# Kernel optimization log

Measured on AMD Instinct MI355X. Metric: run time of the kernel, lower is better.

Reference implementation:

```python
import jax, jax.numpy as jnp
import numpy as np

B, L, D = 4, 4096, 256


def setup_inputs() -> dict:
    key = jax.random.key(0)
    k_x, k_q, k_k, k_v, k_w, k_b = jax.random.split(key, 6)
    s = 1.0 / np.sqrt(D)
    return {
        "x": jax.random.normal(k_x, (B, L, D), dtype=jnp.float32),
        "Wq": jax.random.normal(k_q, (D, D), dtype=jnp.float32) * s,   # nn.Linear weight (out,in)
        "Wk": jax.random.normal(k_k, (D, D), dtype=jnp.float32) * s,
        "Wv": jax.random.normal(k_v, (D, D), dtype=jnp.float32) * s,
        "w_mlp": jax.random.normal(k_w, (D,), dtype=jnp.float32) * s,  # Linear(D,1) weight
        "b_mlp": jnp.zeros((), dtype=jnp.float32),                     # Linear(D,1) bias
    }


def reference(x, Wq, Wk, Wv, w_mlp, b_mlp):
    # Projections (nn.Linear: y = x @ W.T, no bias)
    Q = jnp.einsum("bld,ed->ble", x, Wq)
    K = jnp.einsum("bld,ed->ble", x, Wk)
    V = jnp.einsum("bld,ed->ble", x, Wv)
    # score[b,i,j] = relu((Q[b,i]-K[b,j]) @ w_mlp + b_mlp)
    # decomposed: (Q-K)@w = Q@w - K@w  (exact same math, no (B,L,L,D) tensor)
    q_s = Q @ w_mlp  # (B,L)
    k_s = K @ w_mlp  # (B,L)
    scores = jax.nn.relu(q_s[:, :, None] - k_s[:, None, :] + b_mlp)  # (B,L,L)
    attn = jax.nn.softmax(scores, axis=-1)  # softmax over key axis j
    # out[b,i,d] = sum_j attn[b,i,j] * V[b,j,d]
    out = jnp.einsum("bij,bjd->bid", attn, V)
    return out  # dropout p=0.0 is identity
```

## Files before the change

### kernel.cpp

```cpp
#include <hip/hip_runtime.h>
#include <math.h>

#define BB 4
#define LL 4096
#define DD 256
#define NROWS (BB*LL)
#define CHUNK 32
#define NC (LL/CHUNK)
#define NB 8192

typedef __bf16 bf16x8 __attribute__((ext_vector_type(8)));
typedef __bf16 bf16x4 __attribute__((ext_vector_type(4)));
typedef float floatx4 __attribute__((ext_vector_type(4)));

__global__ void k_prep(const float* __restrict__ Wq, const float* __restrict__ Wk,
                       const float* __restrict__ Wv, const float* __restrict__ w,
                       float* __restrict__ u,
                       __bf16* __restrict__ Wh, __bf16* __restrict__ Wl) {
    __shared__ float wl[16];
    int d = threadIdx.x;
    int e0 = blockIdx.x * 16;
    if (d < 16) wl[d] = w[e0 + d];
    __syncthreads();
    float aq = 0.f, ak = 0.f;
    #pragma unroll
    for (int j = 0; j < 16; ++j) {
        float we = wl[j];
        aq = fmaf(Wq[(size_t)(e0 + j)*DD + d], we, aq);
        ak = fmaf(Wk[(size_t)(e0 + j)*DD + d], we, ak);
        float wv = Wv[(size_t)(e0 + j)*DD + d];
        __bf16 h = (__bf16)wv;
        Wh[(size_t)(e0 + j)*DD + d] = h;
        Wl[(size_t)(e0 + j)*DD + d] = (__bf16)(wv - (float)h);
    }
    atomicAdd(&u[d], aq);
    atomicAdd(&u[DD + d], ak);
}

__global__ void __launch_bounds__(256) k_gemm_mfma(
        const float* __restrict__ x,
        const __bf16* __restrict__ Wh, const __bf16* __restrict__ Wl,
        const float* __restrict__ u, const float* __restrict__ bmlp,
        float* __restrict__ V, float* __restrict__ a, float* __restrict__ c) {
    __shared__ __bf16 Ah[32*40];
    __shared__ __bf16 Al[32*40];
    __shared__ float4 ul[128];
    __shared__ float pros[512];
    const int tid = threadIdx.x;
    const int wave = tid >> 6, lane = tid & 63;
    const int rowBase = blockIdx.x * 32;
    const int quad = lane >> 4, l16 = lane & 15;
    const int srow = tid >> 3, skq = (tid & 7) * 4;

    if (tid < 128) ul[tid] = ((const float4*)u)[tid];

    floatx4 acc[2][4];
    #pragma unroll
    for (int rt = 0; rt < 2; ++rt)
        #pragma unroll
        for (int ct = 0; ct < 4; ++ct)
            acc[rt][ct] = (floatx4){0.f, 0.f, 0.f, 0.f};
    float aq = 0.f, ak = 0.f;

    for (int k0 = 0; k0 < DD; k0 += 32) {
        __syncthreads();
        float4 xv = *(const float4*)(x + (size_t)(rowBase + srow)*DD + k0 + skq);
        __bf16 h0 = (__bf16)xv.x, h1 = (__bf16)xv.y, h2 = (__bf16)xv.z, h3 = (__bf16)xv.w;
        bf16x4 hv = {h0, h1, h2, h3};
        bf16x4 lv = {(__bf16)(xv.x - (float)h0), (__bf16)(xv.y - (float)h1),
                     (__bf16)(xv.z - (float)h2), (__bf16)(xv.w - (float)h3)};
        *(bf16x4*)&Ah[srow*40 + skq] = hv;
        *(bf16x4*)&Al[srow*40 + skq] = lv;
        float4 q4 = ul[(k0 >> 2) + (tid & 7)];
        float4 k4 = ul[64 + (k0 >> 2) + (tid & 7)];
        aq = fmaf(xv.x, q4.x, fmaf(xv.y, q4.y, fmaf(xv.z, q4.z, fmaf(xv.w, q4.w, aq))));
        ak = fmaf(xv.x, k4.x, fmaf(xv.y, k4.y, fmaf(xv.z, k4.z, fmaf(xv.w, k4.w, ak))));
        __syncthreads();
        bf16x8 ah[2], al[2];
        #pragma unroll
        for (int rt = 0; rt < 2; ++rt) {
            int m = rt*16 + l16;
            ah[rt] = *(bf16x8*)&Ah[m*40 + quad*8];
            al[rt] = *(bf16x8*)&Al[m*40 + quad*8];
        }
        #pragma unroll
        for (int ct = 0; ct < 4; ++ct) {
            int n = wave*64 + ct*16 + l16;
            bf16x8 bh = *(const bf16x8*)(Wh + (size_t)n*DD + k0 + quad*8);
            bf16x8 bl = *(const bf16x8*)(Wl + (size_t)n*DD + k0 + quad*8);
            #pragma unroll
            for (int rt = 0; rt < 2; ++rt) {
                acc[rt][ct] = __builtin_amdgcn_mfma_f32_16x16x32_bf16(ah[rt], bh, acc[rt][ct], 0, 0, 0);
                acc[rt][ct] = __builtin_amdgcn_mfma_f32_16x16x32_bf16(ah[rt], bl, acc[rt][ct], 0, 0, 0);
                acc[rt][ct] = __builtin_amdgcn_mfma_f32_16x16x32_bf16(al[rt], bh, acc[rt][ct], 0, 0, 0);
            }
        }
    }
    #pragma unroll
    for (int rt = 0; rt < 2; ++rt)
        #pragma unroll
        for (int ct = 0; ct < 4; ++ct)
            #pragma unroll
            for (int i = 0; i < 4; ++i) {
                int row = rowBase + rt*16 + quad*4 + i;
                int col = wave*64 + ct*16 + l16;
                V[(size_t)row*DD + col] = acc[rt][ct][i];
            }
    __syncthreads();
    pros[tid] = aq;
    pros[256 + tid] = ak;
    __syncthreads();
    if (tid < 32) {
        float sa = 0.f, sc = 0.f;
        #pragma unroll
        for (int j = 0; j < 8; ++j) {
            sa += pros[tid*8 + j];
            sc += pros[256 + tid*8 + j];
        }
        a[rowBase + tid] = sa + bmlp[0];
        c[rowBase + tid] = sc;
    }
}

__global__ void __launch_bounds__(1024) k_sortish(const float* __restrict__ c,
        int* __restrict__ binstart_g, int* __restrict__ perm,
        float* __restrict__ c_sorted, float* __restrict__ e_sorted,
        float* __restrict__ SE, float* __restrict__ hdr) {
    __shared__ float cl[LL];
    __shared__ int   hist[NB];
    __shared__ float esl[LL];
    __shared__ float scrf[64];
    int b = blockIdx.x, tid = threadIdx.x;
    int wave = tid >> 6, lane = tid & 63;
    int* scri = (int*)scrf;

    float4 cv = ((const float4*)(c + (size_t)b*LL))[tid];
    ((float4*)cl)[tid] = cv;
    float cw[4] = {cv.x, cv.y, cv.z, cv.w};
    float mn = fminf(fminf(cw[0],cw[1]), fminf(cw[2],cw[3]));
    float mx = fmaxf(fmaxf(cw[0],cw[1]), fmaxf(cw[2],cw[3]));
    #pragma unroll
    for (int off = 32; off > 0; off >>= 1) {
        mn = fminf(mn, __shfl_down(mn, off));
        mx = fmaxf(mx, __shfl_down(mx, off));
    }
    if (lane == 0) { scrf[wave] = mn; scrf[32 + wave] = mx; }
    __syncthreads();
    if (wave == 0) {
        float m = (lane < 16) ? scrf[lane]      :  3.4e38f;
        float M = (lane < 16) ? scrf[32 + lane] : -3.4e38f;
        #pragma unroll
        for (int off = 32; off > 0; off >>= 1) {
            m = fminf(m, __shfl_down(m, off));
            M = fmaxf(M, __shfl_down(M, off));
        }
        if (lane == 0) { scrf[0] = m; scrf[1] = M; }
    }
    __syncthreads();
    float cmin = scrf[0], cmax = scrf[1];
    float scale = (float)NB / fmaxf(cmax - cmin, 1e-20f);
    __syncthreads();

    ((int4*)hist)[tid] = make_int4(0,0,0,0);
    ((int4*)hist)[tid + 1024] = make_int4(0,0,0,0);
    __syncthreads();

    int bins[4];
    #pragma unroll
    for (int u = 0; u < 4; ++u) {
        int bi = (int)((cw[u] - cmin) * scale);
        bi = bi < 0 ? 0 : (bi > NB-1 ? NB-1 : bi);
        bins[u] = bi;
        atomicAdd(&hist[bi], 1);
    }
    __syncthreads();

    int loc[8]; int base = 0;
    #pragma unroll
    for (int j = 0; j < 8; ++j) { loc[j] = base; base += hist[tid*8 + j]; }
    int incl = base;
    #pragma unroll
    for (int off = 1; off < 64; off <<= 1) {
        int t = __shfl_up(incl, off);
        if (lane >= off) incl += t;
    }
    if (lane == 63) scri[wave] = incl;
    __syncthreads();
    if (wave == 0) {
        int v = (lane < 16) ? scri[lane] : 0;
        int s = v;
        #pragma unroll
        for (int off = 1; off < 16; off <<= 1) {
            int t = __shfl_up(s, off);
            if (lane >= off) s += t;
        }
        if (lane < 16) scri[lane] = s - v;
    }
    __syncthreads();
    int thread_excl = (incl - base) + scri[wave];
    __syncthreads();
    #pragma unroll
    for (int j = 0; j < 8; ++j) {
        int bs = thread_excl + loc[j];
        binstart_g[(size_t)b*(NB+2) + tid*8 + j] = bs;
        hist[tid*8 + j] = bs;
    }
    if (tid == 0) {
        binstart_g[(size_t)b*(NB+2) + NB]     = LL;
        binstart_g[(size_t)b*(NB+2) + NB + 1] = LL;
        hdr[b*2 + 0] = cmin;
        hdr[b*2 + 1] = scale;
    }
    __syncthreads();

    #pragma unroll
    for (int u = 0; u < 4; ++u) {
        int i = tid*4 + u;
        int r = atomicAdd(&hist[bins[u]], 1);
        float e = expf(cmin - cw[u]);
        perm[(size_t)b*LL + r] = i;
        c_sorted[(size_t)b*LL + r] = cw[u];
        e_sorted[(size_t)b*LL + r] = e;
        esl[r] = e;
    }
    __syncthreads();

    float le[4]; float s0 = 0.f;
    #pragma unroll
    for (int u = 0; u < 4; ++u) { le[u] = s0; s0 += esl[tid*4 + u]; }
    float fincl = s0;
    #pragma unroll
    for (int off = 1; off < 64; off <<= 1) {
        float t = __shfl_up(fincl, off);
        if (lane >= off) fincl += t;
    }
    if (lane == 63) scrf[wave] = fincl;
    __syncthreads();
    if (wave == 0) {
        float v = (lane < 16) ? scrf[lane] : 0.f;
        float s = v;
        #pragma unroll
        for (int off = 1; off < 16; off <<= 1) {
            float t = __shfl_up(s, off);
            if (lane >= off) s += t;
        }
        if (lane < 16) scrf[lane] = s - v;
    }
    __syncthreads();
    float texcl = (fincl - s0) + scrf[wave];
    #pragma unroll
    for (int u = 0; u < 4; ++u)
        SE[(size_t)b*(LL+1) + tid*4 + u] = texcl + le[u];
    if (tid == 1023) SE[(size_t)b*(LL+1) + LL] = texcl + s0;
}

__global__ void k_scan(const float* __restrict__ V, const int* __restrict__ perm,
        const float* __restrict__ e_sorted,
        float* __restrict__ Pl, float* __restrict__ Pel,
        float* __restrict__ Tp, float* __restrict__ Te) {
    int b = blockIdx.y, q = blockIdx.x;
    int d = threadIdx.x;
    __shared__ int pj[CHUNK];
    __shared__ float pe[CHUNK];
    if (d < CHUNK) {
        pj[d] = perm[(size_t)b*LL + q*CHUNK + d];
        pe[d] = e_sorted[(size_t)b*LL + q*CHUNK + d];
    }
    __syncthreads();
    float vr[CHUNK];
    #pragma unroll
    for (int r = 0; r < CHUNK; ++r)
        vr[r] = V[((size_t)b*LL + pj[r]) * DD + d];
    float acc = 0.f, acce = 0.f;
    size_t kb = (size_t)b*LL + (size_t)q*CHUNK;
    #pragma unroll
    for (int r = 0; r < CHUNK; ++r) {
        size_t o = (kb + r) * DD + d;
        Pl[o]  = acc;
        Pel[o] = acce;
        acc += vr[r];
        acce = fmaf(pe[r], vr[r], acce);
    }
    size_t to = ((size_t)b*NC + q) * DD + d;
    Tp[to] = acc;
    Te[to] = acce;
}

__global__ void k_base(const float* __restrict__ Tp, const float* __restrict__ Te,
        float* __restrict__ baseP, float* __restrict__ basePe) {
    int q = blockIdx.x, b = blockIdx.y, d = threadIdx.x;
    float acc = 0.f, acce = 0.f;
    #pragma unroll 8
    for (int i = 0; i < q; ++i) {
        size_t ti = ((size_t)b*NC + i) * DD + d;
        acc += Tp[ti]; acce += Te[ti];
    }
    size_t o = ((size_t)b*(NC+1) + q) * DD + d;
    baseP[o] = acc; basePe[o] = acce;
}

__global__ void k_out(const float* __restrict__ a, const float* __restrict__ hdr,
                      const int* __restrict__ binstart,
                      const float* __restrict__ c_sorted, const float* __restrict__ e_sorted,
                      const int* __restrict__ perm, const float* __restrict__ V,
                      const float* __restrict__ SE,
                      const float* __restrict__ Pl, const float* __restrict__ Pel,
                      const float* __restrict__ baseP, const float* __restrict__ basePe,
                      float* __restrict__ out) {
    int row = blockIdx.x * 4 + (threadIdx.x >> 6);
    int lane = threadIdx.x & 63;
    int b = row >> 12;
    float ai = a[row];
    float cmin = hdr[b*2 + 0], scale = hdr[b*2 + 1];
    float t = (ai - cmin) * scale;
    int ib = t < 0.f ? 0 : (t >= (float)NB ? NB : (int)t);
    int k    = binstart[(size_t)b*(NB+2) + ib];
    int kend = binstart[(size_t)b*(NB+2) + ib + 1];
    float alpha = expf(cmin - ai);
    float Z = fmaf(alpha, (float)(LL - k), SE[(size_t)b*(LL+1) + k]);
    size_t db = (size_t)lane * 4;
    size_t totoff = ((size_t)b * (NC+1) + NC) * DD + db;
    float4 ptot  = *(const float4*)(baseP  + totoff);
    float4 pk, pek;
    if (k < LL) {
        int q = k >> 5;
        size_t po = ((size_t)b * LL + k) * DD + db;
        size_t bo = ((size_t)b * (NC+1) + q) * DD + db;
        float4 pl = *(const float4*)(Pl    + po);
        float4 bp = *(const float4*)(baseP + bo);
        float4 pe = *(const float4*)(Pel    + po);
        float4 be = *(const float4*)(basePe + bo);
        pk.x = pl.x + bp.x; pk.y = pl.y + bp.y; pk.z = pl.z + bp.z; pk.w = pl.w + bp.w;
        pek.x = pe.x + be.x; pek.y = pe.y + be.y; pek.z = pe.z + be.z; pek.w = pe.w + be.w;
    } else {
        pk = ptot;
        float4 pt = *(const float4*)(basePe + totoff);
        pek = pt;
    }
    float4 num;
    num.x = fmaf(alpha, ptot.x - pk.x, pek.x);
    num.y = fmaf(alpha, ptot.y - pk.y, pek.y);
    num.z = fmaf(alpha, ptot.z - pk.z, pek.z);
    num.w = fmaf(alpha, ptot.w - pk.w, pek.w);
    for (int r = k; r < kend; ++r) {
        float cr = c_sorted[(size_t)b*LL + r];
        if (cr < ai) {
            float w = e_sorted[(size_t)b*LL + r] - alpha;
            int j = perm[(size_t)b*LL + r];
            float4 v = *(const float4*)(V + ((size_t)b*LL + j) * DD + db);
            num.x = fmaf(w, v.x, num.x);
            num.y = fmaf(w, v.y, num.y);
            num.z = fmaf(w, v.z, num.z);
            num.w = fmaf(w, v.w, num.w);
            Z += w;
        }
    }
    float invZ = 1.f / Z;
    float4 o;
    o.x = num.x * invZ; o.y = num.y * invZ; o.z = num.z * invZ; o.w = num.w * invZ;
    *(float4*)(out + (size_t)row * DD + db) = o;
}

extern "C" void kernel_launch(void* const* d_in, const int* in_sizes, int n_in,
                              void* d_out, int out_size, void* d_ws, size_t ws_size,
                              hipStream_t stream) {
    const float* x  = (const float*)d_in[0];
    const float* Wq = (const float*)d_in[1];
    const float* Wk = (const float*)d_in[2];
    const float* Wv = (const float*)d_in[3];
    const float* wm = (const float*)d_in[4];
    const float* bm = (const float*)d_in[5];
    float* out = (float*)d_out;
    float* ws = (float*)d_ws;

    size_t off = 0;
    auto alloc = [&](size_t n) {
        float* p = ws + off;
        off += (n + 255) & ~(size_t)255;
        return p;
    };
    float* u        = alloc(2*DD);
    float* a        = alloc(NROWS);
    float* c        = alloc(NROWS);
    float* c_sorted = alloc(NROWS);
    float* e_sorted = alloc(NROWS);
    float* SE       = alloc((size_t)BB*(LL+1));
    int*   perm     = (int*)alloc(NROWS);
    int*   binstart = (int*)alloc((size_t)BB*(NB+2));
    float* hdr      = alloc(2*BB);
    float* V        = alloc((size_t)NROWS*DD);
    float* Pl       = alloc((size_t)NROWS*DD);
    float* Pel      = alloc((size_t)NROWS*DD);
    float* Tp       = alloc((size_t)BB*NC*DD);
    float* Te       = alloc((size_t)BB*NC*DD);
    float* baseP    = alloc((size_t)BB*(NC+1)*DD);
    float* basePe   = alloc((size_t)BB*(NC+1)*DD);
    __bf16* Wh      = (__bf16*)alloc((size_t)DD*DD/2);
    __bf16* Wl      = (__bf16*)alloc((size_t)DD*DD/2);

    hipMemsetAsync(u, 0, 2*DD*sizeof(float), stream);
    hipLaunchKernelGGL(k_prep, dim3(16), dim3(DD), 0, stream, Wq, Wk, Wv, wm, u, Wh, Wl);
    hipLaunchKernelGGL(k_gemm_mfma, dim3(NROWS/32), dim3(256), 0, stream,
                       x, Wh, Wl, u, bm, V, a, c);
    hipLaunchKernelGGL(k_sortish, dim3(BB), dim3(1024), 0, stream,
                       c, binstart, perm, c_sorted, e_sorted, SE, hdr);
    hipLaunchKernelGGL(k_scan, dim3(NC, BB), dim3(DD), 0, stream, V, perm, e_sorted, Pl, Pel, Tp, Te);
    hipLaunchKernelGGL(k_base, dim3(NC+1, BB), dim3(DD), 0, stream, Tp, Te, baseP, basePe);
    hipLaunchKernelGGL(k_out, dim3(NROWS/4), dim3(256), 0, stream,
                       a, hdr, binstart, c_sorted, e_sorted, perm, V,
                       SE, Pl, Pel, baseP, basePe, out);
}
```

Baseline: 137.5 us.

## Fuse scan, base and output kernels with grid barriers; restructure prep and GEMM

Merges the scan, chunk-base and output kernels into one persistent 512-block kernel that uses atomic-counter grid barriers between phases, removing two launches. The prep kernel now reduces the u vectors through shared memory instead of atomics, which drops the memset of u. The GEMM loads x straight into registers in MFMA fragment layout rather than staging it through LDS, and only wave 0 computes the score dot products, reduced with shuffles. The grid barrier relies on all 512 blocks being co-resident and adds spin-wait cost.

```diff
diff --git a/kernel.cpp b/kernel.cpp
--- a/kernel.cpp
+++ b/kernel.cpp
@@ -8,51 +8,66 @@
 #define CHUNK 32
 #define NC (LL/CHUNK)
 #define NB 8192
+#define PBLK 512
 
 typedef __bf16 bf16x8 __attribute__((ext_vector_type(8)));
-typedef __bf16 bf16x4 __attribute__((ext_vector_type(4)));
 typedef float floatx4 __attribute__((ext_vector_type(4)));
 
-__global__ void k_prep(const float* __restrict__ Wq, const float* __restrict__ Wk,
-                       const float* __restrict__ Wv, const float* __restrict__ w,
-                       float* __restrict__ u,
-                       __bf16* __restrict__ Wh, __bf16* __restrict__ Wl) {
-    __shared__ float wl[16];
-    int d = threadIdx.x;
-    int e0 = blockIdx.x * 16;
-    if (d < 16) wl[d] = w[e0 + d];
-    __syncthreads();
-    float aq = 0.f, ak = 0.f;
-    #pragma unroll
-    for (int j = 0; j < 16; ++j) {
-        float we = wl[j];
-        aq = fmaf(Wq[(size_t)(e0 + j)*DD + d], we, aq);
-        ak = fmaf(Wk[(size_t)(e0 + j)*DD + d], we, ak);
-        float wv = Wv[(size_t)(e0 + j)*DD + d];
-        __bf16 h = (__bf16)wv;
-        Wh[(size_t)(e0 + j)*DD + d] = h;
-        Wl[(size_t)(e0 + j)*DD + d] = (__bf16)(wv - (float)h);
-    }
-    atomicAdd(&u[d], aq);
-    atomicAdd(&u[DD + d], ak);
-}
-
-__global__ void __launch_bounds__(256) k_gemm_mfma(
-        const float* __restrict__ x,
+__global__ void __launch_bounds__(256) k_prep(const float* __restrict__ Wq,
+        const float* __restrict__ Wk, const float* __restrict__ Wv,
+        const float* __restrict__ w, float* __restrict__ u,
+        __bf16* __restrict__ Wh, __bf16* __restrict__ Wl) {
+    __shared__ float pq[256*17];
+    __shared__ float pk[256*17];
+    __shared__ float rq[16*17], rk[16*17];
+    int e = threadIdx.x;
+    int d0 = blockIdx.x * 16;
+    float we = w[e];
+    #pragma unroll
+    for (int j4 = 0; j4 < 4; ++j4) {
+        float4 q4 = *(const float4*)(Wq + (size_t)e*DD + d0 + j4*4);
+        float4 k4 = *(const float4*)(Wk + (size_t)e*DD + d0 + j4*4);
+        float4 v4 = *(const float4*)(Wv + (size_t)e*DD + d0 + j4*4);
+        float qa[4] = {q4.x, q4.y, q4.z, q4.w};
+        float ka[4] = {k4.x, k4.y, k4.z, k4.w};
+        float va[4] = {v4.x, v4.y, v4.z, v4.w};
+        #pragma unroll
+        for (int j = 0; j < 4; ++j) {
+            pq[e*17 + j4*4 + j] = qa[j] * we;
+            pk[e*17 + j4*4 + j] = ka[j] * we;
+            __bf16 h = (__bf16)va[j];
+            Wh[(size_t)e*DD + d0 + j4*4 + j] = h;
+            Wl[(size_t)e*DD + d0 + j4*4 + j] = (__bf16)(va[j] - (float)h);
+        }
+    }
+    __syncthreads();
+    int d = e & 15, g = e >> 4;
+    float sq = 0.f, sk = 0.f;
+    #pragma unroll
+    for (int i = 0; i < 16; ++i) {
+        sq += pq[(g*16 + i)*17 + d];
+        sk += pk[(g*16 + i)*17 + d];
+    }
+    rq[g*17 + d] = sq;
+    rk[g*17 + d] = sk;
+    __syncthreads();
+    if (e < 16) {
+        float s1 = 0.f, s2 = 0.f;
+        #pragma unroll
+        for (int gg = 0; gg < 16; ++gg) { s1 += rq[gg*17 + e]; s2 += rk[gg*17 + e]; }
+        u[d0 + e] = s1;
+        u[DD + d0 + e] = s2;
+    }
+}
+
+__global__ void __launch_bounds__(256) k_gemm(const float* __restrict__ x,
         const __bf16* __restrict__ Wh, const __bf16* __restrict__ Wl,
         const float* __restrict__ u, const float* __restrict__ bmlp,
         float* __restrict__ V, float* __restrict__ a, float* __restrict__ c) {
-    __shared__ __bf16 Ah[32*40];
-    __shared__ __bf16 Al[32*40];
-    __shared__ float4 ul[128];
-    __shared__ float pros[512];
     const int tid = threadIdx.x;
     const int wave = tid >> 6, lane = tid & 63;
+    const int quad = lane >> 4, l16 = lane & 15;
     const int rowBase = blockIdx.x * 32;
-    const int quad = lane >> 4, l16 = lane & 15;
-    const int srow = tid >> 3, skq = (tid & 7) * 4;
-
-    if (tid < 128) ul[tid] = ((const float4*)u)[tid];
 
     floatx4 acc[2][4];
     #pragma unroll
@@ -60,34 +75,46 @@
         #pragma unroll
         for (int ct = 0; ct < 4; ++ct)
             acc[rt][ct] = (floatx4){0.f, 0.f, 0.f, 0.f};
-    float aq = 0.f, ak = 0.f;
-
+    float aq0 = 0.f, aq1 = 0.f, ak0 = 0.f, ak1 = 0.f;
+
+    #pragma unroll 1
     for (int k0 = 0; k0 < DD; k0 += 32) {
-        __syncthreads();
-        float4 xv = *(const float4*)(x + (size_t)(rowBase + srow)*DD + k0 + skq);
-        __bf16 h0 = (__bf16)xv.x, h1 = (__bf16)xv.y, h2 = (__bf16)xv.z, h3 = (__bf16)xv.w;
-        bf16x4 hv = {h0, h1, h2, h3};
-        bf16x4 lv = {(__bf16)(xv.x - (float)h0), (__bf16)(xv.y - (float)h1),
-                     (__bf16)(xv.z - (float)h2), (__bf16)(xv.w - (float)h3)};
-        *(bf16x4*)&Ah[srow*40 + skq] = hv;
-        *(bf16x4*)&Al[srow*40 + skq] = lv;
-        float4 q4 = ul[(k0 >> 2) + (tid & 7)];
-        float4 k4 = ul[64 + (k0 >> 2) + (tid & 7)];
-        aq = fmaf(xv.x, q4.x, fmaf(xv.y, q4.y, fmaf(xv.z, q4.z, fmaf(xv.w, q4.w, aq))));
-        ak = fmaf(xv.x, k4.x, fmaf(xv.y, k4.y, fmaf(xv.z, k4.z, fmaf(xv.w, k4.w, ak))));
-        __syncthreads();
+        const int kq = k0 + quad*8;
         bf16x8 ah[2], al[2];
+        float4 x0[2], x1[2];
         #pragma unroll
         for (int rt = 0; rt < 2; ++rt) {
-            int m = rt*16 + l16;
-            ah[rt] = *(bf16x8*)&Ah[m*40 + quad*8];
-            al[rt] = *(bf16x8*)&Al[m*40 + quad*8];
+            const float* xp = x + (size_t)(rowBase + rt*16 + l16)*DD + kq;
+            x0[rt] = *(const float4*)xp;
+            x1[rt] = *(const float4*)(xp + 4);
+            float xs[8] = {x0[rt].x, x0[rt].y, x0[rt].z, x0[rt].w,
+                           x1[rt].x, x1[rt].y, x1[rt].z, x1[rt].w};
+            #pragma unroll
+            for (int j = 0; j < 8; ++j) {
+                __bf16 h = (__bf16)xs[j];
+                ah[rt][j] = h;
+                al[rt][j] = (__bf16)(xs[j] - (float)h);
+            }
+        }
+        if (wave == 0) {
+            float4 uq0 = *(const float4*)(u + kq);
+            float4 uq1 = *(const float4*)(u + kq + 4);
+            float4 uk0 = *(const float4*)(u + DD + kq);
+            float4 uk1 = *(const float4*)(u + DD + kq + 4);
+            aq0 += x0[0].x*uq0.x + x0[0].y*uq0.y + x0[0].z*uq0.z + x0[0].w*uq0.w
+                 + x1[0].x*uq1.x + x1[0].y*uq1.y + x1[0].z*uq1.z + x1[0].w*uq1.w;
+            aq1 += x0[1].x*uq0.x + x0[1].y*uq0.y + x0[1].z*uq0.z + x0[1].w*uq0.w
+                 + x1[1].x*uq1.x + x1[1].y*uq1.y + x1[1].z*uq1.z + x1[1].w*uq1.w;
+            ak0 += x0[0].x*uk0.x + x0[0].y*uk0.y + x0[0].z*uk0.z + x0[0].w*uk0.w
+                 + x1[0].x*uk1.x + x1[0].y*uk1.y + x1[0].z*uk1.z + x1[0].w*uk1.w;
+            ak1 += x0[1].x*uk0.x + x0[1].y*uk0.y + x0[1].z*uk0.z + x0[1].w*uk0.w
+                 + x1[1].x*uk1.x + x1[1].y*uk1.y + x1[1].z*uk1.z + x1[1].w*uk1.w;
         }
         #pragma unroll
         for (int ct = 0; ct < 4; ++ct) {
             int n = wave*64 + ct*16 + l16;
-            bf16x8 bh = *(const bf16x8*)(Wh + (size_t)n*DD + k0 + quad*8);
-            bf16x8 bl = *(const bf16x8*)(Wl + (size_t)n*DD + k0 + quad*8);
+            bf16x8 bh = *(const bf16x8*)(Wh + (size_t)n*DD + kq);
+            bf16x8 bl = *(const bf16x8*)(Wl + (size_t)n*DD + kq);
             #pragma unroll
             for (int rt = 0; rt < 2; ++rt) {
                 acc[rt][ct] = __builtin_amdgcn_mfma_f32_16x16x32_bf16(ah[rt], bh, acc[rt][ct], 0, 0, 0);
@@ -101,24 +128,21 @@
         #pragma unroll
         for (int ct = 0; ct < 4; ++ct)
             #pragma unroll
-            for (int i = 0; i < 4; ++i) {
-                int row = rowBase + rt*16 + quad*4 + i;
-                int col = wave*64 + ct*16 + l16;
-                V[(size_t)row*DD + col] = acc[rt][ct][i];
-            }
-    __syncthreads();
-    pros[tid] = aq;
-    pros[256 + tid] = ak;
-    __syncthreads();
-    if (tid < 32) {
-        float sa = 0.f, sc = 0.f;
-        #pragma unroll
-        for (int j = 0; j < 8; ++j) {
-            sa += pros[tid*8 + j];
-            sc += pros[256 + tid*8 + j];
-        }
-        a[rowBase + tid] = sa + bmlp[0];
-        c[rowBase + tid] = sc;
+            for (int i = 0; i < 4; ++i)
+                V[(size_t)(rowBase + rt*16 + quad*4 + i)*DD + wave*64 + ct*16 + l16]
+                    = acc[rt][ct][i];
+    if (wave == 0) {
+        aq0 += __shfl_xor(aq0, 16); aq0 += __shfl_xor(aq0, 32);
+        aq1 += __shfl_xor(aq1, 16); aq1 += __shfl_xor(aq1, 32);
+        ak0 += __shfl_xor(ak0, 16); ak0 += __shfl_xor(ak0, 32);
+        ak1 += __shfl_xor(ak1, 16); ak1 += __shfl_xor(ak1, 32);
+        if (lane < 16) {
+            float bias = bmlp[0];
+            a[rowBase + lane]      = aq0 + bias;
+            a[rowBase + 16 + lane] = aq1 + bias;
+            c[rowBase + lane]      = ak0;
+            c[rowBase + 16 + lane] = ak1;
+        }
     }
 }
 
@@ -254,111 +278,124 @@
     if (tid == 1023) SE[(size_t)b*(LL+1) + LL] = texcl + s0;
 }
 
-__global__ void k_scan(const float* __restrict__ V, const int* __restrict__ perm,
+__device__ __forceinline__ void grid_barrier(int* cnt, int expected) {
+    __syncthreads();
+    if (threadIdx.x == 0) {
+        __threadfence();
+        atomicAdd(cnt, 1);
+        while (atomicAdd(cnt, 0) < expected) { __builtin_amdgcn_s_sleep(4); }
+        __threadfence();
+    }
+    __syncthreads();
+}
+
+__global__ void __launch_bounds__(256) k_post(
+        const float* __restrict__ V, const int* __restrict__ perm,
         const float* __restrict__ e_sorted,
         float* __restrict__ Pl, float* __restrict__ Pel,
-        float* __restrict__ Tp, float* __restrict__ Te) {
-    int b = blockIdx.y, q = blockIdx.x;
-    int d = threadIdx.x;
+        float* __restrict__ Tp, float* __restrict__ Te,
+        float* __restrict__ baseP, float* __restrict__ basePe,
+        const float* __restrict__ a, const float* __restrict__ hdr,
+        const int* __restrict__ binstart, const float* __restrict__ c_sorted,
+        const float* __restrict__ SE, float* __restrict__ out,
+        int* __restrict__ bar) {
     __shared__ int pj[CHUNK];
     __shared__ float pe[CHUNK];
-    if (d < CHUNK) {
-        pj[d] = perm[(size_t)b*LL + q*CHUNK + d];
-        pe[d] = e_sorted[(size_t)b*LL + q*CHUNK + d];
-    }
-    __syncthreads();
-    float vr[CHUNK];
-    #pragma unroll
-    for (int r = 0; r < CHUNK; ++r)
-        vr[r] = V[((size_t)b*LL + pj[r]) * DD + d];
-    float acc = 0.f, acce = 0.f;
-    size_t kb = (size_t)b*LL + (size_t)q*CHUNK;
-    #pragma unroll
-    for (int r = 0; r < CHUNK; ++r) {
-        size_t o = (kb + r) * DD + d;
-        Pl[o]  = acc;
-        Pel[o] = acce;
-        acc += vr[r];
-        acce = fmaf(pe[r], vr[r], acce);
-    }
-    size_t to = ((size_t)b*NC + q) * DD + d;
-    Tp[to] = acc;
-    Te[to] = acce;
-}
-
-__global__ void k_base(const float* __restrict__ Tp, const float* __restrict__ Te,
-        float* __restrict__ baseP, float* __restrict__ basePe) {
-    int q = blockIdx.x, b = blockIdx.y, d = threadIdx.x;
-    float acc = 0.f, acce = 0.f;
-    #pragma unroll 8
-    for (int i = 0; i < q; ++i) {
-        size_t ti = ((size_t)b*NC + i) * DD + d;
-        acc += Tp[ti]; acce += Te[ti];
-    }
-    size_t o = ((size_t)b*(NC+1) + q) * DD + d;
-    baseP[o] = acc; basePe[o] = acce;
-}
-
-__global__ void k_out(const float* __restrict__ a, const float* __restrict__ hdr,
-                      const int* __restrict__ binstart,
-                      const float* __restrict__ c_sorted, const float* __restrict__ e_sorted,
-                      const int* __restrict__ perm, const float* __restrict__ V,
-                      const float* __restrict__ SE,
-                      const float* __restrict__ Pl, const float* __restrict__ Pel,
-                      const float* __restrict__ baseP, const float* __restrict__ basePe,
-                      float* __restrict__ out) {
-    int row = blockIdx.x * 4 + (threadIdx.x >> 6);
-    int lane = threadIdx.x & 63;
-    int b = row >> 12;
-    float ai = a[row];
-    float cmin = hdr[b*2 + 0], scale = hdr[b*2 + 1];
-    float t = (ai - cmin) * scale;
-    int ib = t < 0.f ? 0 : (t >= (float)NB ? NB : (int)t);
-    int k    = binstart[(size_t)b*(NB+2) + ib];
-    int kend = binstart[(size_t)b*(NB+2) + ib + 1];
-    float alpha = expf(cmin - ai);
-    float Z = fmaf(alpha, (float)(LL - k), SE[(size_t)b*(LL+1) + k]);
-    size_t db = (size_t)lane * 4;
-    size_t totoff = ((size_t)b * (NC+1) + NC) * DD + db;
-    float4 ptot  = *(const float4*)(baseP  + totoff);
-    float4 pk, pek;
-    if (k < LL) {
-        int q = k >> 5;
-        size_t po = ((size_t)b * LL + k) * DD + db;
-        size_t bo = ((size_t)b * (NC+1) + q) * DD + db;
-        float4 pl = *(const float4*)(Pl    + po);
-        float4 bp = *(const float4*)(baseP + bo);
-        float4 pe = *(const float4*)(Pel    + po);
-        float4 be = *(const float4*)(basePe + bo);
-        pk.x = pl.x + bp.x; pk.y = pl.y + bp.y; pk.z = pl.z + bp.z; pk.w = pl.w + bp.w;
-        pek.x = pe.x + be.x; pek.y = pe.y + be.y; pek.z = pe.z + be.z; pek.w = pe.w + be.w;
-    } else {
-        pk = ptot;
-        float4 pt = *(const float4*)(basePe + totoff);
-        pek = pt;
-    }
-    float4 num;
-    num.x = fmaf(alpha, ptot.x - pk.x, pek.x);
-    num.y = fmaf(alpha, ptot.y - pk.y, pek.y);
-    num.z = fmaf(alpha, ptot.z - pk.z, pek.z);
-    num.w = fmaf(alpha, ptot.w - pk.w, pek.w);
-    for (int r = k; r < kend; ++r) {
-        float cr = c_sorted[(size_t)b*LL + r];
-        if (cr < ai) {
-            float w = e_sorted[(size_t)b*LL + r] - alpha;
-            int j = perm[(size_t)b*LL + r];
-            float4 v = *(const float4*)(V + ((size_t)b*LL + j) * DD + db);
-            num.x = fmaf(w, v.x, num.x);
-            num.y = fmaf(w, v.y, num.y);
-            num.z = fmaf(w, v.z, num.z);
-            num.w = fmaf(w, v.w, num.w);
-            Z += w;
-        }
-    }
-    float invZ = 1.f / Z;
-    float4 o;
-    o.x = num.x * invZ; o.y = num.y * invZ; o.z = num.z * invZ; o.w = num.w * invZ;
-    *(float4*)(out + (size_t)row * DD + db) = o;
+    const int bid = blockIdx.x, tid = threadIdx.x;
+
+    {
+        int q = bid & (NC-1), b = bid >> 7;
+        int d = tid;
+        if (d < CHUNK) {
+            pj[d] = perm[(size_t)b*LL + q*CHUNK + d];
+            pe[d] = e_sorted[(size_t)b*LL + q*CHUNK + d];
+        }
+        __syncthreads();
+        float vr[CHUNK];
+        #pragma unroll
+        for (int r = 0; r < CHUNK; ++r)
+            vr[r] = V[((size_t)b*LL + pj[r]) * DD + d];
+        float acc = 0.f, acce = 0.f;
+        size_t kb = (size_t)b*LL + (size_t)q*CHUNK;
+        #pragma unroll
+        for (int r = 0; r < CHUNK; ++r) {
+            size_t o = (kb + r) * DD + d;
+            Pl[o]  = acc;
+            Pel[o] = acce;
+            acc += vr[r];
+            acce = fmaf(pe[r], vr[r], acce);
+        }
+        size_t to = ((size_t)b*NC + q) * DD + d;
+        Tp[to] = acc;
+        Te[to] = acce;
+    }
+    grid_barrier(&bar[0], PBLK);
+
+    for (int t = bid; t < (NC+1)*BB; t += PBLK) {
+        int q = t >> 2, b = t & 3;
+        float acc = 0.f, acce = 0.f;
+        for (int i = 0; i < q; ++i) {
+            size_t ti = ((size_t)b*NC + i) * DD + tid;
+            acc += Tp[ti]; acce += Te[ti];
+        }
+        size_t o = ((size_t)b*(NC+1) + q) * DD + tid;
+        baseP[o] = acc; basePe[o] = acce;
+    }
+    grid_barrier(&bar[1], PBLK);
+
+    for (int t = bid; t < NROWS/4; t += PBLK) {
+        int row = t*4 + (tid >> 6);
+        int lane = tid & 63;
+        int b = row >> 12;
+        float ai = a[row];
+        float cmin = hdr[b*2 + 0], scale = hdr[b*2 + 1];
+        float tt = (ai - cmin) * scale;
+        int ib = tt < 0.f ? 0 : (tt >= (float)NB ? NB : (int)tt);
+        int k    = binstart[(size_t)b*(NB+2) + ib];
+        int kend = binstart[(size_t)b*(NB+2) + ib + 1];
+        float alpha = expf(cmin - ai);
+        float Z = fmaf(alpha, (float)(LL - k), SE[(size_t)b*(LL+1) + k]);
+        size_t db = (size_t)lane * 4;
+        size_t totoff = ((size_t)b * (NC+1) + NC) * DD + db;
+        float4 ptot = *(const float4*)(baseP + totoff);
+        float4 pk, pek;
+        if (k < LL) {
+            int q = k >> 5;
+            size_t po = ((size_t)b * LL + k) * DD + db;
+            size_t bo = ((size_t)b * (NC+1) + q) * DD + db;
+            float4 pl = *(const float4*)(Pl    + po);
+            float4 bp = *(const float4*)(baseP + bo);
+            float4 pe4 = *(const float4*)(Pel    + po);
+            float4 be = *(const float4*)(basePe + bo);
+            pk.x = pl.x + bp.x; pk.y = pl.y + bp.y; pk.z = pl.z + bp.z; pk.w = pl.w + bp.w;
+            pek.x = pe4.x + be.x; pek.y = pe4.y + be.y; pek.z = pe4.z + be.z; pek.w = pe4.w + be.w;
+        } else {
+            pk = ptot;
+            pek = *(const float4*)(basePe + totoff);
+        }
+        float4 num;
+        num.x = fmaf(alpha, ptot.x - pk.x, pek.x);
+        num.y = fmaf(alpha, ptot.y - pk.y, pek.y);
+        num.z = fmaf(alpha, ptot.z - pk.z, pek.z);
+        num.w = fmaf(alpha, ptot.w - pk.w, pek.w);
+        for (int r = k; r < kend; ++r) {
+            float cr = c_sorted[(size_t)b*LL + r];
+            if (cr < ai) {
+                float w = e_sorted[(size_t)b*LL + r] - alpha;
+                int j = perm[(size_t)b*LL + r];
+                float4 v = *(const float4*)(V + ((size_t)b*LL + j) * DD + db);
+                num.x = fmaf(w, v.x, num.x);
+                num.y = fmaf(w, v.y, num.y);
+                num.z = fmaf(w, v.z, num.z);
+                num.w = fmaf(w, v.w, num.w);
+                Z += w;
+            }
+        }
+        float invZ = 1.f / Z;
+        float4 o;
+        o.x = num.x * invZ; o.y = num.y * invZ; o.z = num.z * invZ; o.w = num.w * invZ;
+        *(float4*)(out + (size_t)row * DD + db) = o;
+    }
 }
 
 extern "C" void kernel_launch(void* const* d_in, const int* in_sizes, int n_in,
@@ -397,16 +434,15 @@
     float* basePe   = alloc((size_t)BB*(NC+1)*DD);
     __bf16* Wh      = (__bf16*)alloc((size_t)DD*DD/2);
     __bf16* Wl      = (__bf16*)alloc((size_t)DD*DD/2);
-
-    hipMemsetAsync(u, 0, 2*DD*sizeof(float), stream);
-    hipLaunchKernelGGL(k_prep, dim3(16), dim3(DD), 0, stream, Wq, Wk, Wv, wm, u, Wh, Wl);
-    hipLaunchKernelGGL(k_gemm_mfma, dim3(NROWS/32), dim3(256), 0, stream,
+    int*   bar      = (int*)alloc(64);
+
+    hipMemsetAsync(bar, 0, 2*sizeof(int), stream);
+    hipLaunchKernelGGL(k_prep, dim3(16), dim3(256), 0, stream, Wq, Wk, Wv, wm, u, Wh, Wl);
+    hipLaunchKernelGGL(k_gemm, dim3(NROWS/32), dim3(256), 0, stream,
                        x, Wh, Wl, u, bm, V, a, c);
     hipLaunchKernelGGL(k_sortish, dim3(BB), dim3(1024), 0, stream,
                        c, binstart, perm, c_sorted, e_sorted, SE, hdr);
-    hipLaunchKernelGGL(k_scan, dim3(NC, BB), dim3(DD), 0, stream, V, perm, e_sorted, Pl, Pel, Tp, Te);
-    hipLaunchKernelGGL(k_base, dim3(NC+1, BB), dim3(DD), 0, stream, Tp, Te, baseP, basePe);
-    hipLaunchKernelGGL(k_out, dim3(NROWS/4), dim3(256), 0, stream,
-                       a, hdr, binstart, c_sorted, e_sorted, perm, V,
-                       SE, Pl, Pel, baseP, basePe, out);
-}
+    hipLaunchKernelGGL(k_post, dim3(PBLK), dim3(256), 0, stream,
+                       V, perm, e_sorted, Pl, Pel, Tp, Te, baseP, basePe,
+                       a, hdr, binstart, c_sorted, SE, out, bar);
+}
```

Measured after the change: 278.6 us. +102.7%, slower.
